# Optimization experiments

Measured on AMD Instinct MI355X. Metric: run time of the kernel, lower is better.

## Reference

```python
import jax, jax.numpy as jnp
import numpy as np

N, P, D = 262144, 128, 64
EPS = 1e-5
NEG = -1e30


def setup_inputs() -> dict:
    key = jax.random.key(0)
    ks = jax.random.split(key, 12)
    feature = jax.random.normal(ks[0], (N, D), jnp.float32)
    feature_geo = jax.random.normal(ks[1], (N, D), jnp.float32)
    xyz = jax.random.uniform(ks[2], (N, 3), jnp.float32)
    centers = jax.random.uniform(ks[3], (3,), jnp.float32)
    plane_center = jax.random.uniform(ks[4], (P, 3), jnp.float32)
    nrm = jax.random.normal(ks[5], (P, 3), jnp.float32)
    plane_normal = nrm / jnp.linalg.norm(nrm, axis=1, keepdims=True)
    lo = 0.3 * jax.random.uniform(ks[6], (P, 3), jnp.float32)
    hi = 0.5 + 0.5 * jax.random.uniform(ks[7], (P, 3), jnp.float32)
    # exactly two active axes per plane (one axis of the aabb is zeroed)
    ax = jnp.arange(P) % 3
    keep = (jnp.arange(3)[None, :] != ax[:, None]).astype(jnp.float32)
    plane_xyz_min = lo * keep
    plane_xyz_max = hi * keep
    w1 = 0.05 * jax.random.normal(ks[8], (2 * D, D), jnp.float32)
    b1 = jnp.zeros((D,), jnp.float32)
    w2 = 0.05 * jax.random.normal(ks[9], (D, D), jnp.float32)
    b2 = jnp.zeros((D,), jnp.float32)
    w3 = 0.05 * jax.random.normal(ks[10], (D, 1), jnp.float32)
    b3 = jnp.zeros((1,), jnp.float32)
    g1 = jnp.ones((D,), jnp.float32); be1 = jnp.zeros((D,), jnp.float32)
    m1 = jnp.zeros((D,), jnp.float32); v1 = jnp.ones((D,), jnp.float32)
    g2 = jnp.ones((D,), jnp.float32); be2 = jnp.zeros((D,), jnp.float32)
    m2 = jnp.zeros((D,), jnp.float32); v2 = jnp.ones((D,), jnp.float32)
    return dict(feature=feature, feature_geo=feature_geo, xyz=xyz, centers=centers,
                plane_center=plane_center, plane_normal=plane_normal,
                plane_xyz_min=plane_xyz_min, plane_xyz_max=plane_xyz_max,
                w1=w1, b1=b1, g1=g1, be1=be1, m1=m1, v1=v1,
                w2=w2, b2=b2, g2=g2, be2=be2, m2=m2, v2=v2,
                w3=w3, b3=b3)


def _bn(x, g, b, m, v):
    return (x - m) * (g * jax.lax.rsqrt(v + EPS)) + b


def reference(feature, feature_geo, xyz, centers, plane_center, plane_normal,
              plane_xyz_min, plane_xyz_max, w1, b1, g1, be1, m1, v1,
              w2, b2, g2, be2, m2, v2, w3, b3):
    clouds = xyz + centers                                   # [N,3]
    f = jnp.concatenate([feature, feature_geo], axis=1)      # [N,2D]
    # 1x1 conv MLP == per-point matmul (fc1 -> fc2 with BN+ReLU, fc3)
    h1 = jax.nn.relu(_bn(f @ w1 + b1, g1, be1, m1, v1))      # [N,D]
    h2 = jax.nn.relu(_bn(h1 @ w2 + b2, g2, be2, m2, v2))     # [N,D]
    scores = jax.nn.relu(h2 @ w3 + b3)[:, 0]                 # [N]
    # per-plane aabb mask over the two active axes (xyz_max != 0)
    active = plane_xyz_max != 0                              # [P,3]
    in_rng = (clouds[None] >= plane_xyz_min[:, None]) & (clouds[None] < plane_xyz_max[:, None])
    range_mask = jnp.all(in_rng | ~active[:, None, :], axis=-1)   # [P,N]
    # point-to-plane distance: |(clouds - center) . normal|
    dots = clouds @ plane_normal.T                           # [N,P]
    offs = jnp.sum(plane_center * plane_normal, axis=1)      # [P]
    dist = jnp.abs(dots - offs[None, :]).T                   # [P,N]
    mask = range_mask & (dist < 0.1)                         # [P,N]
    sig = jax.nn.sigmoid(scores)                             # [N]
    on_mask = mask & (sig > 0.5)[None, :]
    off_mask = mask & (sig <= 0.5)[None, :]

    def pool(m):  # masked max-pool of fc2 features over points of one plane
        val = jnp.max(jnp.where(m[:, None], h2, NEG), axis=0)     # [D]
        return jnp.where(jnp.any(m), val, 0.0)

    on_feat = jax.lax.map(pool, on_mask)                     # [P,D]
    off_feat = jax.lax.map(pool, off_mask)                   # [P,D]
    scores_masked = jnp.where(mask, scores[None, :], 0.0)    # [P,N]
    return scores_masked, mask, on_mask, off_mask, on_feat, off_feat
```

## Files before the change

kernel.cpp:

```cpp
#include <hip/hip_runtime.h>
#include <hip/hip_bf16.h>
#include <math.h>

#define NPTS 262144
#define NP   128
#define DD   64
#define NWORDS (NPTS / 64)

__global__ __launch_bounds__(256) void prep_kernel(
    const float* __restrict__ plane_center, const float* __restrict__ plane_normal,
    const float* __restrict__ pmin, const float* __restrict__ pmax,
    float* __restrict__ packed, float* __restrict__ out_feats)
{
    const int t = threadIdx.x;
    out_feats[blockIdx.x * 256 + t] = 0.0f;
    if (blockIdx.x == 0 && t < NP) {
        float n0 = plane_normal[t*3+0], n1 = plane_normal[t*3+1], n2 = plane_normal[t*3+2];
        float c0 = plane_center[t*3+0], c1 = plane_center[t*3+1], c2 = plane_center[t*3+2];
        float off = (c0*n0 + c1*n1) + c2*n2;
        float4* pp = reinterpret_cast<float4*>(packed) + t * 3;
        pp[0] = make_float4(n0, n1, n2, off);
        pp[1] = make_float4(pmin[t*3+0], pmin[t*3+1], pmin[t*3+2], 0.0f);
        pp[2] = make_float4(pmax[t*3+0], pmax[t*3+1], pmax[t*3+2], 0.0f);
    }
}

__global__ __launch_bounds__(256, 4) void fused_kernel(
    const float* __restrict__ feature, const float* __restrict__ feature_geo,
    const float* __restrict__ xyz, const float* __restrict__ centers,
    const float* __restrict__ packed,
    const float* __restrict__ w1, const float* __restrict__ b1,
    const float* __restrict__ g1, const float* __restrict__ be1,
    const float* __restrict__ m1, const float* __restrict__ v1,
    const float* __restrict__ w2, const float* __restrict__ b2,
    const float* __restrict__ g2, const float* __restrict__ be2,
    const float* __restrict__ m2, const float* __restrict__ v2,
    const float* __restrict__ w3, const float* __restrict__ b3,
    float* __restrict__ h2_out,
    float* __restrict__ out_sm, float* __restrict__ out_mask,
    float* __restrict__ out_on, float* __restrict__ out_off,
    unsigned long long* __restrict__ hitOn, unsigned long long* __restrict__ hitOff)
{
    const int t = threadIdx.x;
    const int n = blockIdx.x * 256 + t;
    const int lane = t & 63;
    const int word = n >> 6;

    const float c0 = xyz[n*3+0] + centers[0];
    const float c1 = xyz[n*3+1] + centers[1];
    const float c2 = xyz[n*3+2] + centers[2];

    const float4* pp = reinterpret_cast<const float4*>(packed);
    unsigned long long mklo = 0ull, mkhi = 0ull;

    float acc[DD];
#pragma unroll
    for (int j = 0; j < DD; ++j) acc[j] = 0.0f;

    const float4* fA = reinterpret_cast<const float4*>(feature) + (size_t)n * 16;
    const float4* fB = reinterpret_cast<const float4*>(feature_geo) + (size_t)n * 16;
#pragma unroll 1
    for (int q = 0; q < 16; ++q) {
        const float4 fv = fA[q];
        const float* wr = w1 + q * 4 * DD;
#pragma unroll
        for (int j = 0; j < DD; ++j) acc[j] = fmaf(fv.x, wr[j], acc[j]);
#pragma unroll
        for (int j = 0; j < DD; ++j) acc[j] = fmaf(fv.y, wr[DD + j], acc[j]);
#pragma unroll
        for (int j = 0; j < DD; ++j) acc[j] = fmaf(fv.z, wr[2 * DD + j], acc[j]);
#pragma unroll
        for (int j = 0; j < DD; ++j) acc[j] = fmaf(fv.w, wr[3 * DD + j], acc[j]);
#pragma unroll
        for (int u = 0; u < 4; ++u) {
            const int p = q * 4 + u;
            const float4 nrm = pp[p*3+0];
            const float4 mn  = pp[p*3+1];
            const float4 mx  = pp[p*3+2];
            float d = fabsf(fmaf(c2, nrm.z, fmaf(c1, nrm.y, c0 * nrm.x)) - nrm.w);
            bool ok0 = (mx.x == 0.0f) | ((c0 >= mn.x) & (c0 < mx.x));
            bool ok1 = (mx.y == 0.0f) | ((c1 >= mn.y) & (c1 < mx.y));
            bool ok2 = (mx.z == 0.0f) | ((c2 >= mn.z) & (c2 < mx.z));
            bool mk  = ok0 & ok1 & ok2 & (d < 0.1f);
            __builtin_nontemporal_store(mk ? 1.0f : 0.0f, &out_mask[(size_t)p * NPTS + n]);
            mklo |= ((unsigned long long)mk) << p;
        }
    }
    const float* w1b = w1 + DD * DD;
#pragma unroll 1
    for (int q = 0; q < 16; ++q) {
        const float4 fv = fB[q];
        const float* wr = w1b + q * 4 * DD;
#pragma unroll
        for (int j = 0; j < DD; ++j) acc[j] = fmaf(fv.x, wr[j], acc[j]);
#pragma unroll
        for (int j = 0; j < DD; ++j) acc[j] = fmaf(fv.y, wr[DD + j], acc[j]);
#pragma unroll
        for (int j = 0; j < DD; ++j) acc[j] = fmaf(fv.z, wr[2 * DD + j], acc[j]);
#pragma unroll
        for (int j = 0; j < DD; ++j) acc[j] = fmaf(fv.w, wr[3 * DD + j], acc[j]);
#pragma unroll
        for (int u = 0; u < 4; ++u) {
            const int p = 64 + q * 4 + u;
            const float4 nrm = pp[p*3+0];
            const float4 mn  = pp[p*3+1];
            const float4 mx  = pp[p*3+2];
            float d = fabsf(fmaf(c2, nrm.z, fmaf(c1, nrm.y, c0 * nrm.x)) - nrm.w);
            bool ok0 = (mx.x == 0.0f) | ((c0 >= mn.x) & (c0 < mx.x));
            bool ok1 = (mx.y == 0.0f) | ((c1 >= mn.y) & (c1 < mx.y));
            bool ok2 = (mx.z == 0.0f) | ((c2 >= mn.z) & (c2 < mx.z));
            bool mk  = ok0 & ok1 & ok2 & (d < 0.1f);
            __builtin_nontemporal_store(mk ? 1.0f : 0.0f, &out_mask[(size_t)p * NPTS + n]);
            mkhi |= ((unsigned long long)mk) << (p - 64);
        }
    }
    float h1[DD];
#pragma unroll
    for (int j = 0; j < DD; ++j) {
        float sc = g1[j] * (1.0f / sqrtf(v1[j] + 1e-5f));
        float h  = fmaf(acc[j] + b1[j] - m1[j], sc, be1[j]);
        h1[j] = fmaxf(h, 0.0f);
    }

    float s = 0.0f;
    float4* o = reinterpret_cast<float4*>(h2_out) + (size_t)n * 16;
#pragma unroll 1
    for (int hh = 0; hh < 2; ++hh) {
        float a2[32];
#pragma unroll
        for (int j = 0; j < 32; ++j) a2[j] = 0.0f;
        const float* w2h = w2 + hh * 32;
#pragma unroll 1
        for (int q = 0; q < 16; ++q) {
            const float fx = h1[4*q+0], fy = h1[4*q+1], fz = h1[4*q+2], fw = h1[4*q+3];
            const float* wr = w2h + q * 4 * DD;
#pragma unroll
            for (int j = 0; j < 32; ++j) a2[j] = fmaf(fx, wr[j], a2[j]);
#pragma unroll
            for (int j = 0; j < 32; ++j) a2[j] = fmaf(fy, wr[DD + j], a2[j]);
#pragma unroll
            for (int j = 0; j < 32; ++j) a2[j] = fmaf(fz, wr[2 * DD + j], a2[j]);
#pragma unroll
            for (int j = 0; j < 32; ++j) a2[j] = fmaf(fw, wr[3 * DD + j], a2[j]);
        }
#pragma unroll
        for (int j = 0; j < 32; ++j) {
            const int jj = hh * 32 + j;
            float sc = g2[jj] * (1.0f / sqrtf(v2[jj] + 1e-5f));
            float h  = fmaf(a2[j] + b2[jj] - m2[jj], sc, be2[jj]);
            h = fmaxf(h, 0.0f);
            a2[j] = h;
            s = fmaf(h, w3[jj], s);
        }
#pragma unroll
        for (int q = 0; q < 8; ++q)
            o[hh * 8 + q] = make_float4(a2[4*q+0], a2[4*q+1], a2[4*q+2], a2[4*q+3]);
    }
    s += b3[0];
    const float score = fmaxf(s, 0.0f);

    const bool on = (0.5f + 0.5f * tanhf(0.5f * score)) > 0.5f;

#pragma unroll 1
    for (int p = 0; p < 64; ++p) {
        const bool mk = (mklo >> p) & 1ull;
        const size_t idx = (size_t)p * NPTS + n;
        const bool mon  = mk & on;
        const bool moff = mk & (!on);
        __builtin_nontemporal_store(mk ? score : 0.0f, &out_sm[idx]);
        __builtin_nontemporal_store(mon ? 1.0f : 0.0f, &out_on[idx]);
        __builtin_nontemporal_store(moff ? 1.0f : 0.0f, &out_off[idx]);
        unsigned long long bOn  = __ballot(mon);
        unsigned long long bOff = __ballot(moff);
        if (lane == 0) {
            hitOn [(size_t)p * NWORDS + word] = bOn;
            hitOff[(size_t)p * NWORDS + word] = bOff;
        }
    }
#pragma unroll 1
    for (int p = 64; p < 128; ++p) {
        const bool mk = (mkhi >> (p - 64)) & 1ull;
        const size_t idx = (size_t)p * NPTS + n;
        const bool mon  = mk & on;
        const bool moff = mk & (!on);
        __builtin_nontemporal_store(mk ? score : 0.0f, &out_sm[idx]);
        __builtin_nontemporal_store(mon ? 1.0f : 0.0f, &out_on[idx]);
        __builtin_nontemporal_store(moff ? 1.0f : 0.0f, &out_off[idx]);
        unsigned long long bOn  = __ballot(mon);
        unsigned long long bOff = __ballot(moff);
        if (lane == 0) {
            hitOn [(size_t)p * NWORDS + word] = bOn;
            hitOff[(size_t)p * NWORDS + word] = bOff;
        }
    }
}

__global__ __launch_bounds__(256) void pool_kernel(
    const float* __restrict__ h2,
    const unsigned long long* __restrict__ hitOn,
    const unsigned long long* __restrict__ hitOff,
    int* __restrict__ out_feats_i)
{
    __shared__ float tile[128 * DD];
    __shared__ unsigned long long bm[2][NP][2];
    const int t = threadIdx.x;
    const int lane = t & 63;
    const int wv = t >> 6;

    float accOn[32], accOff[32];
#pragma unroll
    for (int i = 0; i < 32; ++i) { accOn[i] = 0.0f; accOff[i] = 0.0f; }

    for (int cc = 0; cc < 4; ++cc) {
        const int chunk = blockIdx.x * 4 + cc;
        const int base  = chunk * 128;
        const float4* src = reinterpret_cast<const float4*>(h2 + (size_t)base * DD);
        float4* dst = reinterpret_cast<float4*>(tile);
#pragma unroll
        for (int q = 0; q < 8; ++q) dst[t + q * 256] = src[t + q * 256];
        {
            const int p = t & 127;
            const int half = t >> 7;
            const unsigned long long* hsrc = half ? hitOff : hitOn;
            const int w0 = chunk * 2;
            bm[half][p][0] = hsrc[(size_t)p * NWORDS + w0 + 0];
            bm[half][p][1] = hsrc[(size_t)p * NWORDS + w0 + 1];
        }
        __syncthreads();

#pragma unroll
        for (int i = 0; i < 32; ++i) {
            const int p = wv * 32 + i;
            unsigned long long m;
            m = bm[0][p][0];
            while (m) { int nn = __builtin_ctzll(m); m &= m - 1;
                        accOn[i]  = fmaxf(accOn[i],  tile[nn * DD + lane]); }
            m = bm[0][p][1];
            while (m) { int nn = __builtin_ctzll(m); m &= m - 1;
                        accOn[i]  = fmaxf(accOn[i],  tile[(64 + nn) * DD + lane]); }
            m = bm[1][p][0];
            while (m) { int nn = __builtin_ctzll(m); m &= m - 1;
                        accOff[i] = fmaxf(accOff[i], tile[nn * DD + lane]); }
            m = bm[1][p][1];
            while (m) { int nn = __builtin_ctzll(m); m &= m - 1;
                        accOff[i] = fmaxf(accOff[i], tile[(64 + nn) * DD + lane]); }
        }
        __syncthreads();
    }
#pragma unroll
    for (int i = 0; i < 32; ++i) {
        const int p = wv * 32 + i;
        if (accOn[i]  != 0.0f) atomicMax(&out_feats_i[p * DD + lane],            __float_as_int(accOn[i]));
        if (accOff[i] != 0.0f) atomicMax(&out_feats_i[NP * DD + p * DD + lane],  __float_as_int(accOff[i]));
    }
}

extern "C" void kernel_launch(void* const* d_in, const int* in_sizes, int n_in,
                              void* d_out, int out_size, void* d_ws, size_t ws_size,
                              hipStream_t stream) {
    const float* feature      = (const float*)d_in[0];
    const float* feature_geo  = (const float*)d_in[1];
    const float* xyz          = (const float*)d_in[2];
    const float* centers      = (const float*)d_in[3];
    const float* plane_center = (const float*)d_in[4];
    const float* plane_normal = (const float*)d_in[5];
    const float* pmin         = (const float*)d_in[6];
    const float* pmax         = (const float*)d_in[7];
    const float* w1 = (const float*)d_in[8];
    const float* b1 = (const float*)d_in[9];
    const float* g1 = (const float*)d_in[10];
    const float* be1 = (const float*)d_in[11];
    const float* m1 = (const float*)d_in[12];
    const float* v1 = (const float*)d_in[13];
    const float* w2 = (const float*)d_in[14];
    const float* b2 = (const float*)d_in[15];
    const float* g2 = (const float*)d_in[16];
    const float* be2 = (const float*)d_in[17];
    const float* m2 = (const float*)d_in[18];
    const float* v2 = (const float*)d_in[19];
    const float* w3 = (const float*)d_in[20];
    const float* b3 = (const float*)d_in[21];

    float* out = (float*)d_out;
    const size_t PN = (size_t)NP * NPTS;
    float* out_sm    = out;
    float* out_mask  = out + PN;
    float* out_on    = out + 2 * PN;
    float* out_off   = out + 3 * PN;
    float* out_feats = out + 4 * PN;

    float* h2     = (float*)d_ws;
    unsigned long long* hitOn  = (unsigned long long*)(h2 + (size_t)NPTS * DD);
    unsigned long long* hitOff = hitOn + (size_t)NP * NWORDS;
    float* packed = (float*)(hitOff + (size_t)NP * NWORDS);

    prep_kernel<<<64, 256, 0, stream>>>(
        plane_center, plane_normal, pmin, pmax, packed, out_feats);
    fused_kernel<<<NPTS / 256, 256, 0, stream>>>(
        feature, feature_geo, xyz, centers, packed,
        w1, b1, g1, be1, m1, v1, w2, b2, g2, be2, m2, v2, w3, b3,
        h2, out_sm, out_mask, out_on, out_off, hitOn, hitOff);
    pool_kernel<<<512, 256, 0, stream>>>(h2, hitOn, hitOff, (int*)out_feats);
}
```

Baseline: 876.8 us.

## Load uniform weights via constant address space and restructure fc2 with transposed weights

Casts the weight, BN-parameter and plane pointers to address space 4 (constant) so the compiler can emit scalar loads instead of per-lane vector loads. The prep kernel now transposes w2 into the workspace, and fc2 is rewritten as per-output dot products over the h1 values held in registers, computing four outputs at a time instead of two 32-wide halves. The min-waves launch bound is dropped, letting the compiler use more registers. This trades possible lower occupancy and a small extra prep step for less vector-memory traffic on uniform weights.

```diff
diff --git a/kernel.cpp b/kernel.cpp
--- a/kernel.cpp
+++ b/kernel.cpp
@@ -7,10 +7,19 @@
 #define DD   64
 #define NWORDS (NPTS / 64)
 
+#define AS4 __attribute__((address_space(4)))
+typedef float evf4 __attribute__((ext_vector_type(4)));
+typedef AS4 const float* csf;
+typedef AS4 const evf4*  csf4;
+#define TO_CSF(p)  ((csf)(unsigned long long)(const void*)(p))
+#define TO_CSF4(p) ((csf4)(unsigned long long)(const void*)(p))
+
 __global__ __launch_bounds__(256) void prep_kernel(
     const float* __restrict__ plane_center, const float* __restrict__ plane_normal,
     const float* __restrict__ pmin, const float* __restrict__ pmax,
-    float* __restrict__ packed, float* __restrict__ out_feats)
+    const float* __restrict__ w2,
+    float* __restrict__ packed, float* __restrict__ w2T,
+    float* __restrict__ out_feats)
 {
     const int t = threadIdx.x;
     out_feats[blockIdx.x * 256 + t] = 0.0f;
@@ -23,16 +32,24 @@
         pp[1] = make_float4(pmin[t*3+0], pmin[t*3+1], pmin[t*3+2], 0.0f);
         pp[2] = make_float4(pmax[t*3+0], pmax[t*3+1], pmax[t*3+2], 0.0f);
     }
+    if (blockIdx.x == 1) {
+#pragma unroll
+        for (int u = 0; u < 16; ++u) {
+            const int e = u * 256 + t;
+            const int j = e >> 6, k = e & 63;
+            w2T[e] = w2[k * DD + j];
+        }
+    }
 }
 
-__global__ __launch_bounds__(256, 4) void fused_kernel(
+__global__ __launch_bounds__(256) void fused_kernel(
     const float* __restrict__ feature, const float* __restrict__ feature_geo,
     const float* __restrict__ xyz, const float* __restrict__ centers,
     const float* __restrict__ packed,
     const float* __restrict__ w1, const float* __restrict__ b1,
     const float* __restrict__ g1, const float* __restrict__ be1,
     const float* __restrict__ m1, const float* __restrict__ v1,
-    const float* __restrict__ w2, const float* __restrict__ b2,
+    const float* __restrict__ w2T, const float* __restrict__ b2,
     const float* __restrict__ g2, const float* __restrict__ be2,
     const float* __restrict__ m2, const float* __restrict__ v2,
     const float* __restrict__ w3, const float* __restrict__ b3,
@@ -46,11 +63,14 @@
     const int lane = t & 63;
     const int word = n >> 6;
 
-    const float c0 = xyz[n*3+0] + centers[0];
-    const float c1 = xyz[n*3+1] + centers[1];
-    const float c2 = xyz[n*3+2] + centers[2];
-
-    const float4* pp = reinterpret_cast<const float4*>(packed);
+    const csf  cc  = TO_CSF(centers);
+    const csf4 pp  = TO_CSF4(packed);
+    const csf  w1c = TO_CSF(w1);
+
+    const float c0 = xyz[n*3+0] + cc[0];
+    const float c1 = xyz[n*3+1] + cc[1];
+    const float c2 = xyz[n*3+2] + cc[2];
+
     unsigned long long mklo = 0ull, mkhi = 0ull;
 
     float acc[DD];
@@ -62,7 +82,7 @@
 #pragma unroll 1
     for (int q = 0; q < 16; ++q) {
         const float4 fv = fA[q];
-        const float* wr = w1 + q * 4 * DD;
+        const csf wr = w1c + q * 4 * DD;
 #pragma unroll
         for (int j = 0; j < DD; ++j) acc[j] = fmaf(fv.x, wr[j], acc[j]);
 #pragma unroll
@@ -74,9 +94,9 @@
 #pragma unroll
         for (int u = 0; u < 4; ++u) {
             const int p = q * 4 + u;
-            const float4 nrm = pp[p*3+0];
-            const float4 mn  = pp[p*3+1];
-            const float4 mx  = pp[p*3+2];
+            const evf4 nrm = pp[p*3+0];
+            const evf4 mn  = pp[p*3+1];
+            const evf4 mx  = pp[p*3+2];
             float d = fabsf(fmaf(c2, nrm.z, fmaf(c1, nrm.y, c0 * nrm.x)) - nrm.w);
             bool ok0 = (mx.x == 0.0f) | ((c0 >= mn.x) & (c0 < mx.x));
             bool ok1 = (mx.y == 0.0f) | ((c1 >= mn.y) & (c1 < mx.y));
@@ -86,11 +106,11 @@
             mklo |= ((unsigned long long)mk) << p;
         }
     }
-    const float* w1b = w1 + DD * DD;
+    const csf w1b = w1c + DD * DD;
 #pragma unroll 1
     for (int q = 0; q < 16; ++q) {
         const float4 fv = fB[q];
-        const float* wr = w1b + q * 4 * DD;
+        const csf wr = w1b + q * 4 * DD;
 #pragma unroll
         for (int j = 0; j < DD; ++j) acc[j] = fmaf(fv.x, wr[j], acc[j]);
 #pragma unroll
@@ -102,9 +122,9 @@
 #pragma unroll
         for (int u = 0; u < 4; ++u) {
             const int p = 64 + q * 4 + u;
-            const float4 nrm = pp[p*3+0];
-            const float4 mn  = pp[p*3+1];
-            const float4 mx  = pp[p*3+2];
+            const evf4 nrm = pp[p*3+0];
+            const evf4 mn  = pp[p*3+1];
+            const evf4 mx  = pp[p*3+2];
             float d = fabsf(fmaf(c2, nrm.z, fmaf(c1, nrm.y, c0 * nrm.x)) - nrm.w);
             bool ok0 = (mx.x == 0.0f) | ((c0 >= mn.x) & (c0 < mx.x));
             bool ok1 = (mx.y == 0.0f) | ((c1 >= mn.y) & (c1 < mx.y));
@@ -114,49 +134,50 @@
             mkhi |= ((unsigned long long)mk) << (p - 64);
         }
     }
-    float h1[DD];
-#pragma unroll
-    for (int j = 0; j < DD; ++j) {
-        float sc = g1[j] * (1.0f / sqrtf(v1[j] + 1e-5f));
-        float h  = fmaf(acc[j] + b1[j] - m1[j], sc, be1[j]);
-        h1[j] = fmaxf(h, 0.0f);
-    }
-
+    {
+        const csf g1c = TO_CSF(g1), v1c = TO_CSF(v1), b1c = TO_CSF(b1),
+                  m1c = TO_CSF(m1), be1c = TO_CSF(be1);
+#pragma unroll
+        for (int j = 0; j < DD; ++j) {
+            float sc = g1c[j] * (1.0f / sqrtf(v1c[j] + 1e-5f));
+            float h  = fmaf(acc[j] + b1c[j] - m1c[j], sc, be1c[j]);
+            acc[j] = fmaxf(h, 0.0f);
+        }
+    }
+
+    const csf w2t = TO_CSF(w2T);
+    const csf g2c = TO_CSF(g2), v2c = TO_CSF(v2), b2c = TO_CSF(b2),
+              m2c = TO_CSF(m2), be2c = TO_CSF(be2), w3c = TO_CSF(w3);
     float s = 0.0f;
     float4* o = reinterpret_cast<float4*>(h2_out) + (size_t)n * 16;
 #pragma unroll 1
-    for (int hh = 0; hh < 2; ++hh) {
-        float a2[32];
-#pragma unroll
-        for (int j = 0; j < 32; ++j) a2[j] = 0.0f;
-        const float* w2h = w2 + hh * 32;
-#pragma unroll 1
-        for (int q = 0; q < 16; ++q) {
-            const float fx = h1[4*q+0], fy = h1[4*q+1], fz = h1[4*q+2], fw = h1[4*q+3];
-            const float* wr = w2h + q * 4 * DD;
-#pragma unroll
-            for (int j = 0; j < 32; ++j) a2[j] = fmaf(fx, wr[j], a2[j]);
-#pragma unroll
-            for (int j = 0; j < 32; ++j) a2[j] = fmaf(fy, wr[DD + j], a2[j]);
-#pragma unroll
-            for (int j = 0; j < 32; ++j) a2[j] = fmaf(fz, wr[2 * DD + j], a2[j]);
-#pragma unroll
-            for (int j = 0; j < 32; ++j) a2[j] = fmaf(fw, wr[3 * DD + j], a2[j]);
-        }
-#pragma unroll
-        for (int j = 0; j < 32; ++j) {
-            const int jj = hh * 32 + j;
-            float sc = g2[jj] * (1.0f / sqrtf(v2[jj] + 1e-5f));
-            float h  = fmaf(a2[j] + b2[jj] - m2[jj], sc, be2[jj]);
+    for (int jq = 0; jq < 16; ++jq) {
+        const csf r0 = w2t + (4*jq + 0) * DD;
+        const csf r1 = w2t + (4*jq + 1) * DD;
+        const csf r2 = w2t + (4*jq + 2) * DD;
+        const csf r3 = w2t + (4*jq + 3) * DD;
+        float a0 = 0.0f, a1 = 0.0f, a2 = 0.0f, a3 = 0.0f;
+#pragma unroll
+        for (int k = 0; k < DD; ++k) {
+            const float h = acc[k];
+            a0 = fmaf(h, r0[k], a0);
+            a1 = fmaf(h, r1[k], a1);
+            a2 = fmaf(h, r2[k], a2);
+            a3 = fmaf(h, r3[k], a3);
+        }
+        float hv[4] = {a0, a1, a2, a3};
+#pragma unroll
+        for (int u = 0; u < 4; ++u) {
+            const int jj = 4*jq + u;
+            float sc = g2c[jj] * (1.0f / sqrtf(v2c[jj] + 1e-5f));
+            float h  = fmaf(hv[u] + b2c[jj] - m2c[jj], sc, be2c[jj]);
             h = fmaxf(h, 0.0f);
-            a2[j] = h;
-            s = fmaf(h, w3[jj], s);
-        }
-#pragma unroll
-        for (int q = 0; q < 8; ++q)
-            o[hh * 8 + q] = make_float4(a2[4*q+0], a2[4*q+1], a2[4*q+2], a2[4*q+3]);
-    }
-    s += b3[0];
+            hv[u] = h;
+            s = fmaf(h, w3c[jj], s);
+        }
+        o[jq] = make_float4(hv[0], hv[1], hv[2], hv[3]);
+    }
+    s += TO_CSF(b3)[0];
     const float score = fmaxf(s, 0.0f);
 
     const bool on = (0.5f + 0.5f * tanhf(0.5f * score)) > 0.5f;
@@ -293,12 +314,13 @@
     unsigned long long* hitOn  = (unsigned long long*)(h2 + (size_t)NPTS * DD);
     unsigned long long* hitOff = hitOn + (size_t)NP * NWORDS;
     float* packed = (float*)(hitOff + (size_t)NP * NWORDS);
+    float* w2T    = packed + NP * 12;
 
     prep_kernel<<<64, 256, 0, stream>>>(
-        plane_center, plane_normal, pmin, pmax, packed, out_feats);
+        plane_center, plane_normal, pmin, pmax, w2, packed, w2T, out_feats);
     fused_kernel<<<NPTS / 256, 256, 0, stream>>>(
         feature, feature_geo, xyz, centers, packed,
-        w1, b1, g1, be1, m1, v1, w2, b2, g2, be2, m2, v2, w3, b3,
+        w1, b1, g1, be1, m1, v1, w2T, b2, g2, be2, m2, v2, w3, b3,
         h2, out_sm, out_mask, out_on, out_off, hitOn, hitOff);
     pool_kernel<<<512, 256, 0, stream>>>(h2, hitOn, hitOff, (int*)out_feats);
 }
```

New measurement: 850.7 us. 1.03x faster.
